# Performance work log

Measured on AMD Instinct MI355X. Metric: run time of the kernel, lower is better.

The kernel has to match this reference:

```python
import jax, jax.numpy as jnp
import numpy as np

B, N, E = 2, 2048, 1024
H, D = 16, 64  # context_dim = H*D = 1024


def setup_inputs() -> dict:
    key = jax.random.key(0)
    ks = jax.random.split(key, 6)
    s = 0.02
    return {
        "input_emb": jax.random.normal(ks[0], (B, N, E), dtype=jnp.float32),
        "Wq": jax.random.normal(ks[1], (E, H * D), dtype=jnp.float32) * s,
        "Wk": jax.random.normal(ks[2], (E, D), dtype=jnp.float32) * s,
        "Wv": jax.random.normal(ks[3], (E, D), dtype=jnp.float32) * s,
        "Wo": jax.random.normal(ks[4], (H * D, H * D), dtype=jnp.float32) * s,
        "bo": jax.random.normal(ks[5], (H * D,), dtype=jnp.float32) * s,
    }


def reference(input_emb, Wq, Wk, Wv, Wo, bo):
    b, n, _ = input_emb.shape
    Q = (input_emb @ Wq).reshape(b, n, H, D)          # (B,N,H,D)
    K = input_emb @ Wk                                 # (B,N,D) shared across heads (MQA)
    V = input_emb @ Wv                                 # (B,N,D)
    # scores: (B,H,N,N); mask is applied before scaling in the torch code,
    # but -inf/scale == -inf so mask-then-scale == scale-then-mask.
    scores = jnp.einsum("bnhd,bmd->bhnm", Q, K) / jnp.sqrt(jnp.float32(D))
    causal = jnp.tril(jnp.ones((n, n), dtype=bool))    # True = keep
    scores = jnp.where(causal[None, None], scores, -jnp.inf)
    weights = jax.nn.softmax(scores, axis=-1)          # dropout rate 0.0 -> identity
    Z = jnp.einsum("bhnm,bmd->bnhd", weights, V).reshape(b, n, H * D)
    return Z @ Wo + bo
```

## Files before the change

kernel.cpp:

```cpp
#include <hip/hip_runtime.h>
#include <hip/hip_bf16.h>


#define NQ 2048
#define BATCH 2
#define HEADS 16
#define HD 64
#define EMB 1024
#define NKV 1152

typedef short s16x8 __attribute__((ext_vector_type(8)));
typedef float f32x4 __attribute__((ext_vector_type(4)));
typedef unsigned int u32x4 __attribute__((ext_vector_type(4)));
typedef unsigned short ushort_t;

__device__ __forceinline__ ushort_t f2bf(float f) {
    unsigned u = __builtin_bit_cast(unsigned, f);
    u += 0x7fff + ((u >> 16) & 1);
    return (ushort_t)(u >> 16);
}

__device__ __forceinline__ void store_out(float* p, float v) { *p = v; }
__device__ __forceinline__ void store_out(ushort_t* p, float v) { *p = f2bf(v); }

#define GL16(g, l)                                                                  \
    __builtin_amdgcn_global_load_lds(                                               \
        (const __attribute__((address_space(1))) unsigned int*)(g),                 \
        (__attribute__((address_space(3))) unsigned int*)(l), 16, 0, 0)

__global__ __launch_bounds__(256) void prep(const float* __restrict__ x,
                                            const float* __restrict__ Wq,
                                            const float* __restrict__ Wk,
                                            const float* __restrict__ Wv,
                                            const float* __restrict__ Wo,
                                            ushort_t* __restrict__ xb,
                                            ushort_t* __restrict__ Wqkv_t,
                                            ushort_t* __restrict__ Wo_t) {
    const int bid = blockIdx.x, t = threadIdx.x;
    if (bid < 4096) {
        const int i = bid * 1024 + t * 4;
        const float4 v = *(const float4*)&x[i];
        ushort_t o[4] = {f2bf(v.x), f2bf(v.y), f2bf(v.z), f2bf(v.w)};
        *(uint2*)&xb[i] = *(uint2*)o;
        return;
    }
    int tb = bid - 4096;
    const float* src; ushort_t* dst; int N, n0, k0;
    if (tb < 1024)      { src = Wq; N = 1024; dst = Wqkv_t;
                          n0 = (tb & 31) * 32; k0 = (tb >> 5) * 32; }
    else if (tb < 1088) { tb -= 1024; src = Wk; N = 64; dst = Wqkv_t + (size_t)1024 * EMB;
                          n0 = (tb & 1) * 32; k0 = (tb >> 1) * 32; }
    else if (tb < 1152) { tb -= 1088; src = Wv; N = 64; dst = Wqkv_t + (size_t)1088 * EMB;
                          n0 = (tb & 1) * 32; k0 = (tb >> 1) * 32; }
    else                { tb -= 1152; src = Wo; N = 1024; dst = Wo_t;
                          n0 = (tb & 31) * 32; k0 = (tb >> 5) * 32; }
    __shared__ float tile[32][33];
    const int tx = t & 31, ty = t >> 5;
#pragma unroll
    for (int i = 0; i < 32; i += 8)
        tile[ty + i][tx] = src[(size_t)(k0 + ty + i) * N + n0 + tx];
    __syncthreads();
#pragma unroll
    for (int i = 0; i < 32; i += 8)
        dst[(size_t)(n0 + ty + i) * EMB + k0 + tx] = f2bf(tile[tx][ty + i]);
}

__device__ __forceinline__ s16x8 frag(const ushort_t* lds, int row, int lc) {
    const int phys = lc ^ (row & 7);
    return *(const s16x8*)&lds[row * 64 + phys * 8];
}

template<bool HAS_BIAS, bool WRITE_VT, typename OutT>
__global__ __launch_bounds__(256, 2) void gemm_bf16(const ushort_t* __restrict__ A,
                                                    const ushort_t* __restrict__ Bt,
                                                    const float* __restrict__ bias,
                                                    OutT* __restrict__ C,
                                                    ushort_t* __restrict__ Vt,
                                                    int M, int N, int K) {
    __shared__ __align__(16) ushort_t Al[2][128 * 64];
    __shared__ __align__(16) ushort_t Bl[2][128 * 64];
    const int t = threadIdx.x;
    const int w = t >> 6, lane = t & 63, quad = lane >> 4, ln = lane & 15;
    const int wm = w >> 1, wn = w & 1;

    const int nwg = gridDim.x * gridDim.y;
    int lin = blockIdx.y * gridDim.x + blockIdx.x;
    lin = (lin & 7) * (nwg >> 3) + (lin >> 3);
    const int bx = lin % gridDim.x, by = lin / gridDim.x;
    const int row0 = by * 128, col0 = bx * 128;

    const ushort_t* pA[4];
    const ushort_t* pB[4];
#pragma unroll
    for (int it = 0; it < 4; ++it) {
        const int u = (w * 4 + it) * 64 + lane;
        const int row = u >> 3, pc = u & 7;
        const int lc = pc ^ (row & 7);
        pA[it] = A + (size_t)(row0 + row) * K + lc * 8;
        pB[it] = Bt + (size_t)(col0 + row) * K + lc * 8;
    }

#define STAGE_AB(la, lb)                                                            \
    {                                                                               \
        _Pragma("unroll")                                                           \
        for (int it = 0; it < 4; ++it) {                                            \
            GL16(pA[it], (la) + (w * 4 + it) * 512);                                \
            GL16(pB[it], (lb) + (w * 4 + it) * 512);                                \
            pA[it] += 64;                                                           \
            pB[it] += 64;                                                           \
        }                                                                           \
    }

    f32x4 acc[4][4] = {};
    const int nk = K >> 6;

    STAGE_AB(Al[0], Bl[0]);
    __syncthreads();

#pragma unroll 1
    for (int ks = 0; ks < nk; ++ks) {
        const int cur = ks & 1;
        if (ks + 1 < nk) STAGE_AB(Al[cur ^ 1], Bl[cur ^ 1]);

        const ushort_t* la = Al[cur];
        const ushort_t* lb = Bl[cur];
        s16x8 af[4][2], bf[4][2];
#pragma unroll
        for (int mt = 0; mt < 4; ++mt) {
            af[mt][0] = frag(la, wm * 64 + mt * 16 + ln, quad);
            af[mt][1] = frag(la, wm * 64 + mt * 16 + ln, 4 + quad);
        }
#pragma unroll
        for (int nt = 0; nt < 4; ++nt) {
            bf[nt][0] = frag(lb, wn * 64 + nt * 16 + ln, quad);
            bf[nt][1] = frag(lb, wn * 64 + nt * 16 + ln, 4 + quad);
        }
#pragma unroll
        for (int mt = 0; mt < 4; ++mt)
#pragma unroll
            for (int nt = 0; nt < 4; ++nt) {
                acc[mt][nt] = __builtin_amdgcn_mfma_f32_16x16x32_bf16(
                    af[mt][0], bf[nt][0], acc[mt][nt], 0, 0, 0);
                acc[mt][nt] = __builtin_amdgcn_mfma_f32_16x16x32_bf16(
                    af[mt][1], bf[nt][1], acc[mt][nt], 0, 0, 0);
            }
        __syncthreads();
    }
#undef STAGE_AB

#pragma unroll
    for (int nt = 0; nt < 4; ++nt) {
        const int col = col0 + wn * 64 + nt * 16 + ln;
        const float bv = HAS_BIAS ? bias[col] : 0.f;
#pragma unroll
        for (int mt = 0; mt < 4; ++mt) {
#pragma unroll
            for (int r = 0; r < 4; ++r) {
                const int row = row0 + wm * 64 + mt * 16 + quad * 4 + r;
                float v = acc[mt][nt][r] + bv;
                if (WRITE_VT && col < 1024) v *= 0.18033688011112043f;
                store_out(&C[(size_t)row * N + col], v);
            }
            if (WRITE_VT && col >= 1088) {
                const int d = col - 1088;
                const int n = row0 + wm * 64 + mt * 16 + quad * 4;
                const int bb = n >> 11, nn = n & 2047;
                ushort_t tmp[4] = {f2bf(acc[mt][nt][0]), f2bf(acc[mt][nt][1]),
                                   f2bf(acc[mt][nt][2]), f2bf(acc[mt][nt][3])};
                *(uint2*)&Vt[((size_t)bb * 64 + d) * NQ + nn] = *(uint2*)tmp;
            }
        }
    }
}

__device__ __forceinline__ void stage_tile(ushort_t* lds, const ushort_t* g,
                                           size_t rstride, int w, int lane) {
#pragma unroll
    for (int it = 0; it < 2; ++it) {
        const int u = (w * 2 + it) * 64 + lane;
        const int row = u >> 3, pc = u & 7;
        const int lc = pc ^ (row & 7);
        GL16(g + (size_t)row * rstride + lc * 8, lds + (size_t)(w * 2 + it) * 512);
    }
}

__device__ __forceinline__ void stage_k(ushort_t* lds, const ushort_t* g,
                                        int w, int lane) {
#pragma unroll
    for (int it = 0; it < 2; ++it) {
        const int u = (w * 2 + it) * 64 + lane;
        const int row = u >> 3, pc = u & 7;
        const int lc = pc ^ (row & 7);
        const int grow = (row & 32) | (((row >> 2) & 3) << 3) |
                         (((row >> 4) & 1) << 2) | (row & 3);
        GL16(g + (size_t)grow * NKV + lc * 8, lds + (size_t)(w * 2 + it) * 512);
    }
}

__global__ __launch_bounds__(256, 4) void attn_mfma(const ushort_t* __restrict__ QKV,
                                                    const ushort_t* __restrict__ Vt,
                                                    ushort_t* __restrict__ Z) {
    const int bid = blockIdx.x;
    const int qt = 31 - (bid >> 5);
    const int b = (bid >> 4) & 1, h = bid & 15;
    const int t = threadIdx.x;
    const int w = t >> 6, lane = t & 63, quad = lane >> 4, ln = lane & 15;

    __shared__ __align__(16) ushort_t Kl[2][64 * 64];
    __shared__ __align__(16) ushort_t Vl[2][64 * 64];

    const ushort_t* Kg = QKV + (size_t)b * NQ * NKV + 1024;
    const ushort_t* Vg = Vt + (size_t)b * 64 * NQ;

    const ushort_t* Qg = QKV + (size_t)(b * NQ + qt * 64 + w * 16 + ln) * NKV + h * HD;
    const s16x8 aQ0 = *(const s16x8*)(Qg + quad * 8);
    const s16x8 aQ1 = *(const s16x8*)(Qg + 32 + quad * 8);

    stage_k(Kl[0], Kg, w, lane);
    stage_tile(Vl[0], Vg, NQ, w, lane);
    __syncthreads();

    f32x4 o[4];
#pragma unroll
    for (int ii = 0; ii < 4; ++ii) o[ii] = f32x4{0.f, 0.f, 0.f, 0.f};
    float mrow = -1e30f, lrow = 0.f;
    const int qrel = w * 16 + ln;

#pragma unroll 1
    for (int jt = 0; jt <= qt; ++jt) {
        const int cur = jt & 1;
        if (jt < qt) {
            stage_k(Kl[cur ^ 1], Kg + (size_t)(jt + 1) * 64 * NKV, w, lane);
            stage_tile(Vl[cur ^ 1], Vg + (jt + 1) * 64, NQ, w, lane);
        }
        const ushort_t* Kc = Kl[cur];
        const ushort_t* Vc = Vl[cur];

        f32x4 s[4];
        __builtin_amdgcn_s_setprio(1);
#pragma unroll
        for (int nt = 0; nt < 4; ++nt) {
            f32x4 acc = f32x4{0.f, 0.f, 0.f, 0.f};
            acc = __builtin_amdgcn_mfma_f32_16x16x32_bf16(
                frag(Kc, nt * 16 + ln, quad), aQ0, acc, 0, 0, 0);
            acc = __builtin_amdgcn_mfma_f32_16x16x32_bf16(
                frag(Kc, nt * 16 + ln, 4 + quad), aQ1, acc, 0, 0, 0);
            s[nt] = acc;
        }
        __builtin_amdgcn_s_setprio(0);

        if (jt == qt) {
#pragma unroll
            for (int nt = 0; nt < 4; ++nt)
#pragma unroll
                for (int r = 0; r < 4; ++r) {
                    const int kv = (nt >> 1) * 32 + quad * 8 + (nt & 1) * 4 + r;
                    if (kv > qrel) s[nt][r] = -1e30f;
                }
        }

        float m0 = fmaxf(fmaxf(s[0][0], s[0][1]), fmaxf(s[0][2], s[0][3]));
        float m1 = fmaxf(fmaxf(s[1][0], s[1][1]), fmaxf(s[1][2], s[1][3]));
        float m2 = fmaxf(fmaxf(s[2][0], s[2][1]), fmaxf(s[2][2], s[2][3]));
        float m3 = fmaxf(fmaxf(s[3][0], s[3][1]), fmaxf(s[3][2], s[3][3]));
        float rmax = fmaxf(fmaxf(m0, m1), fmaxf(m2, m3));
        rmax = fmaxf(rmax, __shfl_xor(rmax, 16));
        rmax = fmaxf(rmax, __shfl_xor(rmax, 32));

        if (!__all(rmax - mrow <= 8.f)) {
            const float mnew = fmaxf(mrow, rmax);
            const float al = __builtin_amdgcn_exp2f(mrow - mnew);
            mrow = mnew;
            lrow *= al;
#pragma unroll
            for (int ntd = 0; ntd < 4; ++ntd)
#pragma unroll
                for (int r = 0; r < 4; ++r) o[ntd][r] *= al;
        }

        float rsum = 0.f;
#pragma unroll
        for (int nt = 0; nt < 4; ++nt)
#pragma unroll
            for (int r = 0; r < 4; ++r) {
                const float pv = __builtin_amdgcn_exp2f(s[nt][r] - mrow);
                s[nt][r] = pv;
                rsum += pv;
            }
        rsum += __shfl_xor(rsum, 16);
        rsum += __shfl_xor(rsum, 32);
        lrow += rsum;

        unsigned pw0[4], pw1[4];
#pragma unroll
        for (int jj = 0; jj < 4; ++jj) {
            const int nt0 = jj >> 1, rr = 2 * (jj & 1);
            asm("v_cvt_pk_bf16_f32 %0, %1, %2"
                : "=v"(pw0[jj]) : "v"(s[nt0][rr]), "v"(s[nt0][rr + 1]));
            asm("v_cvt_pk_bf16_f32 %0, %1, %2"
                : "=v"(pw1[jj]) : "v"(s[2 + nt0][rr]), "v"(s[2 + nt0][rr + 1]));
        }
        const u32x4 q0 = {pw0[0], pw0[1], pw0[2], pw0[3]};
        const u32x4 q1 = {pw1[0], pw1[1], pw1[2], pw1[3]};
        const s16x8 bP0 = __builtin_bit_cast(s16x8, q0);
        const s16x8 bP1 = __builtin_bit_cast(s16x8, q1);

        __builtin_amdgcn_s_setprio(1);
#pragma unroll
        for (int ntd = 0; ntd < 4; ++ntd) {
            o[ntd] = __builtin_amdgcn_mfma_f32_16x16x32_bf16(
                frag(Vc, ntd * 16 + ln, quad), bP0, o[ntd], 0, 0, 0);
            o[ntd] = __builtin_amdgcn_mfma_f32_16x16x32_bf16(
                frag(Vc, ntd * 16 + ln, 4 + quad), bP1, o[ntd], 0, 0, 0);
        }
        __builtin_amdgcn_s_setprio(0);
        __syncthreads();
    }

    const float invl = 1.f / lrow;
    const size_t row = (size_t)(b * NQ + qt * 64 + w * 16 + ln);
#pragma unroll
    for (int ntd = 0; ntd < 4; ++ntd) {
        ushort_t tmp[4];
#pragma unroll
        for (int r = 0; r < 4; ++r) tmp[r] = f2bf(o[ntd][r] * invl);
        *(uint2*)&Z[row * EMB + h * HD + ntd * 16 + quad * 4] = *(uint2*)tmp;
    }
}

extern "C" void kernel_launch(void* const* d_in, const int* in_sizes, int n_in,
                              void* d_out, int out_size, void* d_ws, size_t ws_size,
                              hipStream_t stream) {
    const float* x  = (const float*)d_in[0];
    const float* Wq = (const float*)d_in[1];
    const float* Wk = (const float*)d_in[2];
    const float* Wv = (const float*)d_in[3];
    const float* Wo = (const float*)d_in[4];
    const float* bo = (const float*)d_in[5];
    float* out = (float*)d_out;

    const int M = BATCH * NQ;
    char* ws = (char*)d_ws;
    ushort_t* xb     = (ushort_t*)ws;
    ushort_t* Wqkv_t = (ushort_t*)(ws + (size_t)8  * 1024 * 1024);
    ushort_t* Wo_t   = (ushort_t*)(ws + (size_t)11 * 1024 * 1024);
    ushort_t* QKV    = (ushort_t*)(ws + (size_t)13 * 1024 * 1024);
    ushort_t* Vt     = (ushort_t*)(ws + (size_t)23 * 1024 * 1024);
    ushort_t* Zb     = (ushort_t*)(ws + (size_t)24 * 1024 * 1024);

    prep<<<dim3(6272), dim3(256), 0, stream>>>(x, Wq, Wk, Wv, Wo, xb, Wqkv_t, Wo_t);
    gemm_bf16<false, true, ushort_t><<<dim3(NKV / 128, M / 128), dim3(256), 0, stream>>>(
        xb, Wqkv_t, nullptr, QKV, Vt, M, NKV, EMB);
    attn_mfma<<<dim3(1024), dim3(256), 0, stream>>>(QKV, Vt, Zb);
    gemm_bf16<true, false, float><<<dim3(EMB / 128, M / 128), dim3(256), 0, stream>>>(
        Zb, Wo_t, bo, out, nullptr, M, EMB, EMB);
}
```

Baseline: 160.3 us.

## Fuse fp32-to-bf16 input conversion into QKV GEMM A-tile staging

Removes the separate pass that converts the fp32 input activations to a bf16 buffer. The QKV GEMM now loads fp32 A tiles into registers, converts them with packed bf16 conversion instructions, and writes them to LDS after the MFMA block, while B still uses direct global-to-LDS loads. This avoids writing and then rereading an 8 MB intermediate. In exchange, the GEMM reads twice as many A bytes, each of the 9 column blocks converts the same data again, and register pressure rises from the 32 extra VGPRs held for A.

```diff
diff --git a/kernel.cpp b/kernel.cpp
--- a/kernel.cpp
+++ b/kernel.cpp
@@ -28,23 +28,14 @@
         (const __attribute__((address_space(1))) unsigned int*)(g),                 \
         (__attribute__((address_space(3))) unsigned int*)(l), 16, 0, 0)
 
-__global__ __launch_bounds__(256) void prep(const float* __restrict__ x,
-                                            const float* __restrict__ Wq,
+__global__ __launch_bounds__(256) void prep(const float* __restrict__ Wq,
                                             const float* __restrict__ Wk,
                                             const float* __restrict__ Wv,
                                             const float* __restrict__ Wo,
-                                            ushort_t* __restrict__ xb,
                                             ushort_t* __restrict__ Wqkv_t,
                                             ushort_t* __restrict__ Wo_t) {
-    const int bid = blockIdx.x, t = threadIdx.x;
-    if (bid < 4096) {
-        const int i = bid * 1024 + t * 4;
-        const float4 v = *(const float4*)&x[i];
-        ushort_t o[4] = {f2bf(v.x), f2bf(v.y), f2bf(v.z), f2bf(v.w)};
-        *(uint2*)&xb[i] = *(uint2*)o;
-        return;
-    }
-    int tb = bid - 4096;
+    int tb = blockIdx.x;
+    const int t = threadIdx.x;
     const float* src; ushort_t* dst; int N, n0, k0;
     if (tb < 1024)      { src = Wq; N = 1024; dst = Wqkv_t;
                           n0 = (tb & 31) * 32; k0 = (tb >> 5) * 32; }
@@ -70,8 +61,9 @@
     return *(const s16x8*)&lds[row * 64 + phys * 8];
 }
 
-template<bool HAS_BIAS, bool WRITE_VT, typename OutT>
+template<bool HAS_BIAS, bool WRITE_VT, bool A_FP32, typename OutT>
 __global__ __launch_bounds__(256, 2) void gemm_bf16(const ushort_t* __restrict__ A,
+                                                    const float* __restrict__ Af,
                                                     const ushort_t* __restrict__ Bt,
                                                     const float* __restrict__ bias,
                                                     OutT* __restrict__ C,
@@ -89,38 +81,105 @@
     const int bx = lin % gridDim.x, by = lin / gridDim.x;
     const int row0 = by * 128, col0 = bx * 128;
 
-    const ushort_t* pA[4];
     const ushort_t* pB[4];
 #pragma unroll
     for (int it = 0; it < 4; ++it) {
         const int u = (w * 4 + it) * 64 + lane;
         const int row = u >> 3, pc = u & 7;
         const int lc = pc ^ (row & 7);
-        pA[it] = A + (size_t)(row0 + row) * K + lc * 8;
         pB[it] = Bt + (size_t)(col0 + row) * K + lc * 8;
     }
-
-#define STAGE_AB(la, lb)                                                            \
+    const ushort_t* pA[4];
+    if (!A_FP32) {
+#pragma unroll
+        for (int it = 0; it < 4; ++it) {
+            const int u = (w * 4 + it) * 64 + lane;
+            const int row = u >> 3, pc = u & 7;
+            const int lc = pc ^ (row & 7);
+            pA[it] = A + (size_t)(row0 + row) * K + lc * 8;
+        }
+    }
+    const int arow = t >> 1;
+    const float* pAf[4];
+    int apc[4];
+    if (A_FP32) {
+#pragma unroll
+        for (int i = 0; i < 4; ++i) {
+            apc[i] = (t & 1) * 4 + i;
+            const int lc = apc[i] ^ (arow & 7);
+            pAf[i] = Af + (size_t)(row0 + arow) * K + lc * 8;
+        }
+    }
+
+#define STAGE_B(lb)                                                                 \
+    {                                                                               \
+        _Pragma("unroll")                                                           \
+        for (int it = 0; it < 4; ++it) {                                            \
+            GL16(pB[it], (lb) + (w * 4 + it) * 512);                                \
+            pB[it] += 64;                                                           \
+        }                                                                           \
+    }
+#define STAGE_A_GL(la)                                                              \
     {                                                                               \
         _Pragma("unroll")                                                           \
         for (int it = 0; it < 4; ++it) {                                            \
             GL16(pA[it], (la) + (w * 4 + it) * 512);                                \
-            GL16(pB[it], (lb) + (w * 4 + it) * 512);                                \
             pA[it] += 64;                                                           \
-            pB[it] += 64;                                                           \
+        }                                                                           \
+    }
+#define LOAD_A_F32(regs)                                                            \
+    {                                                                               \
+        _Pragma("unroll")                                                           \
+        for (int i = 0; i < 4; ++i) {                                               \
+            regs[2 * i]     = *(const float4*)(pAf[i]);                             \
+            regs[2 * i + 1] = *(const float4*)(pAf[i] + 4);                         \
+            pAf[i] += 64;                                                           \
+        }                                                                           \
+    }
+#define WRITE_A_F32(la, regs)                                                       \
+    {                                                                               \
+        _Pragma("unroll")                                                           \
+        for (int i = 0; i < 4; ++i) {                                               \
+            unsigned wq[4];                                                         \
+            asm("v_cvt_pk_bf16_f32 %0, %1, %2" : "=v"(wq[0])                        \
+                : "v"(regs[2 * i].x), "v"(regs[2 * i].y));                          \
+            asm("v_cvt_pk_bf16_f32 %0, %1, %2" : "=v"(wq[1])                        \
+                : "v"(regs[2 * i].z), "v"(regs[2 * i].w));                          \
+            asm("v_cvt_pk_bf16_f32 %0, %1, %2" : "=v"(wq[2])                        \
+                : "v"(regs[2 * i + 1].x), "v"(regs[2 * i + 1].y));                  \
+            asm("v_cvt_pk_bf16_f32 %0, %1, %2" : "=v"(wq[3])                        \
+                : "v"(regs[2 * i + 1].z), "v"(regs[2 * i + 1].w));                  \
+            *(u32x4*)&(la)[arow * 64 + apc[i] * 8] = u32x4{wq[0], wq[1],            \
+                                                           wq[2], wq[3]};           \
         }                                                                           \
     }
 
     f32x4 acc[4][4] = {};
     const int nk = K >> 6;
 
-    STAGE_AB(Al[0], Bl[0]);
+    float4 areg[8];
+    if (A_FP32) {
+        LOAD_A_F32(areg);
+        STAGE_B(Bl[0]);
+        WRITE_A_F32(Al[0], areg);
+    } else {
+        STAGE_A_GL(Al[0]);
+        STAGE_B(Bl[0]);
+    }
     __syncthreads();
 
 #pragma unroll 1
     for (int ks = 0; ks < nk; ++ks) {
         const int cur = ks & 1;
-        if (ks + 1 < nk) STAGE_AB(Al[cur ^ 1], Bl[cur ^ 1]);
+        if (ks + 1 < nk) {
+            if (A_FP32) {
+                LOAD_A_F32(areg);
+                STAGE_B(Bl[cur ^ 1]);
+            } else {
+                STAGE_A_GL(Al[cur ^ 1]);
+                STAGE_B(Bl[cur ^ 1]);
+            }
+        }
 
         const ushort_t* la = Al[cur];
         const ushort_t* lb = Bl[cur];
@@ -144,9 +203,16 @@
                 acc[mt][nt] = __builtin_amdgcn_mfma_f32_16x16x32_bf16(
                     af[mt][1], bf[nt][1], acc[mt][nt], 0, 0, 0);
             }
+
+        if (A_FP32 && ks + 1 < nk)
+            WRITE_A_F32(Al[cur ^ 1], areg);
+
         __syncthreads();
     }
-#undef STAGE_AB
+#undef STAGE_B
+#undef STAGE_A_GL
+#undef LOAD_A_F32
+#undef WRITE_A_F32
 
 #pragma unroll
     for (int nt = 0; nt < 4; ++nt) {
@@ -341,17 +407,18 @@
 
     const int M = BATCH * NQ;
     char* ws = (char*)d_ws;
-    ushort_t* xb     = (ushort_t*)ws;
     ushort_t* Wqkv_t = (ushort_t*)(ws + (size_t)8  * 1024 * 1024);
     ushort_t* Wo_t   = (ushort_t*)(ws + (size_t)11 * 1024 * 1024);
     ushort_t* QKV    = (ushort_t*)(ws + (size_t)13 * 1024 * 1024);
     ushort_t* Vt     = (ushort_t*)(ws + (size_t)23 * 1024 * 1024);
     ushort_t* Zb     = (ushort_t*)(ws + (size_t)24 * 1024 * 1024);
 
-    prep<<<dim3(6272), dim3(256), 0, stream>>>(x, Wq, Wk, Wv, Wo, xb, Wqkv_t, Wo_t);
-    gemm_bf16<false, true, ushort_t><<<dim3(NKV / 128, M / 128), dim3(256), 0, stream>>>(
-        xb, Wqkv_t, nullptr, QKV, Vt, M, NKV, EMB);
+    prep<<<dim3(2176), dim3(256), 0, stream>>>(Wq, Wk, Wv, Wo, Wqkv_t, Wo_t);
+    gemm_bf16<false, true, true, ushort_t>
+        <<<dim3(NKV / 128, M / 128), dim3(256), 0, stream>>>(
+            nullptr, x, Wqkv_t, nullptr, QKV, Vt, M, NKV, EMB);
     attn_mfma<<<dim3(1024), dim3(256), 0, stream>>>(QKV, Vt, Zb);
-    gemm_bf16<true, false, float><<<dim3(EMB / 128, M / 128), dim3(256), 0, stream>>>(
-        Zb, Wo_t, bo, out, nullptr, M, EMB, EMB);
-}
+    gemm_bf16<true, false, false, float>
+        <<<dim3(EMB / 128, M / 128), dim3(256), 0, stream>>>(
+            Zb, nullptr, Wo_t, bo, out, nullptr, M, EMB, EMB);
+}
```

Result: slower. 166.6 us (+3.9%).
